# Kernel tuning notes

Hardware: AMD Instinct MI355X
Metric: run time of the kernel (lower is better)

## Reference

```python
import jax, jax.numpy as jnp
import numpy as np

D_MODEL = 1024


def pos_encoding(seq_len, d_model):
    # pos: [S,1], i: [d/2]
    pos = jnp.arange(seq_len, dtype=jnp.float32)[:, None]
    i = jnp.arange(0, d_model, 2, dtype=jnp.float32)
    angle_rates = 1.0 / jnp.power(10000.0, i / d_model)
    angle_rads = pos * angle_rates  # [S, d/2]
    # NOTE: original concatenates sin block then cos block (not interleaved)
    return jnp.concatenate([jnp.sin(angle_rads), jnp.cos(angle_rads)], axis=-1)  # [S, d]


def setup_inputs() -> dict:
    key = jax.random.key(0)
    ks = jax.random.split(key, 4)
    B, S, D = 4, 2048, D_MODEL
    scale = 1.0 / np.sqrt(D)
    x = jax.random.normal(ks[0], (B, S, D), dtype=jnp.float32)
    Wq = jax.random.normal(ks[1], (D, D), dtype=jnp.float32) * scale
    Wk = jax.random.normal(ks[2], (D, D), dtype=jnp.float32) * scale
    Wv = jax.random.normal(ks[3], (D, D), dtype=jnp.float32) * scale
    bq = jnp.zeros((D,), dtype=jnp.float32)
    bk = jnp.zeros((D,), dtype=jnp.float32)
    bv = jnp.zeros((D,), dtype=jnp.float32)
    return {"x": x, "Wq": Wq, "bq": bq, "Wk": Wk, "bk": bk, "Wv": Wv, "bv": bv}


def reference(x, Wq, bq, Wk, bk, Wv, bv):
    B, S, D = x.shape
    pe = pos_encoding(S, D)  # [S, D]
    h = x + pe[None, :, :]
    q = jnp.einsum('bsd,de->bse', h, Wq) + bq
    k = jnp.einsum('bsd,de->bse', h, Wk) + bk
    v = jnp.einsum('bsd,de->bse', h, Wv) + bv
    logits = jnp.einsum('bqd,bkd->bqk', q, k) / jnp.sqrt(jnp.float32(D))
    attn = jax.nn.softmax(logits, axis=-1)
    out = jnp.einsum('bqk,bkd->bqd', attn, v)
    return x + out
```

## Files before the change

### kernel.cpp

```cpp
#include <hip/hip_runtime.h>
#include <stdint.h>


#define AS1(p) ((__attribute__((address_space(1))) void*)(p))
#define AS3(p) ((__attribute__((address_space(3))) void*)(p))

typedef _Float16 f16x8 __attribute__((ext_vector_type(8)));
typedef _Float16 f16x4 __attribute__((ext_vector_type(4)));
typedef float f32x4 __attribute__((ext_vector_type(4)));

__global__ __launch_bounds__(256) void prep(const float* __restrict__ x,
                                            _Float16* __restrict__ h,
                                            const float* __restrict__ Wq,
                                            const float* __restrict__ Wk,
                                            const float* __restrict__ Wv,
                                            _Float16* __restrict__ Wt,
                                            float* __restrict__ rowsum) {
  const int bx = blockIdx.x;
  const int tid = threadIdx.x;
  if (bx < 8192) {
    const size_t e = ((size_t)bx * 256 + tid) * 4;
    const int d = (int)(e & 1023);
    const int s = (int)((e >> 10) & 2047);
    const float4 xv = *(const float4*)(x + e);
    const int half = d >> 9;
    const int j0 = d & 511;
    const float c = -0.017988946039016f;
    f16x4 o;
#pragma unroll
    for (int t = 0; t < 4; t++) {
      const float r = __expf((float)(j0 + t) * c);
      const float a = (float)s * r;
      const float p = half ? __cosf(a) : __sinf(a);
      const float xe = (t == 0) ? xv.x : (t == 1) ? xv.y : (t == 2) ? xv.z : xv.w;
      o[t] = (_Float16)(xe + p);
    }
    *(f16x4*)(h + e) = o;
  } else if (bx < 11264) {
    __shared__ float t[32][33];
    const int w = bx - 8192;
    const int z = w >> 10;
    const int rem = w & 1023;
    const int n0 = (rem & 31) * 32, k0 = (rem >> 5) * 32;
    const float* W = (z == 0) ? Wq : (z == 1) ? Wk : Wv;
    _Float16* o = Wt + (size_t)z * 1048576;
    const int tx = tid & 31, ty = tid >> 5;
#pragma unroll
    for (int i = ty; i < 32; i += 8)
      t[i][tx] = W[(size_t)(k0 + i) * 1024 + (n0 + tx)];
    __syncthreads();
#pragma unroll
    for (int i = ty; i < 32; i += 8)
      o[(size_t)(n0 + i) * 1024 + (k0 + tx)] = (_Float16)t[tx][i];
  } else {
    rowsum[(bx - 11264) * 256 + tid] = 0.f;
  }
}

template <int MODE, int NBUF>
__global__ __launch_bounds__(256) void gemm_bt(
    const _Float16* __restrict__ A0, long long sA,
    const _Float16* __restrict__ B0, long long sB,
    void* __restrict__ C0, long long sC,
    const float* __restrict__ aux0, const float* __restrict__ aux1,
    const float* __restrict__ aux2, float* __restrict__ rowsum,
    _Float16* __restrict__ vT,
    long long sX, const int K, const int N, const int ldc) {
  __shared__ __align__(16) _Float16 As[NBUF * 128 * 32];
  __shared__ __align__(16) _Float16 Bs[NBUF * 128 * 32];
  const int tid = threadIdx.x;
  const int bid = blockIdx.x;

  int z, bm0, bn0;
  if (MODE == 0) {
    const int c = bid & 7, t = bid >> 3;
    const int mhi = t & 7, u = t >> 3;
    bm0 = (mhi * 8 + c) * 128;
    bn0 = (u & 7) * 128;
    z = u >> 3;
  } else if (MODE == 1) {
    const int c = bid & 7, t = bid >> 3;
    const int zx = (t & 7) * 8 + c;
    const int y = t >> 3;
    z = zx >> 4; bm0 = (zx & 15) * 128; bn0 = y * 128;
  } else {
    const int c = bid & 7, t = bid >> 3;
    const int zx = (t & 3) * 8 + c;
    const int y = t >> 2;
    z = zx >> 3; bm0 = (zx & 7) * 128; bn0 = y * 128;
  }
  const _Float16* A = A0 + (size_t)z * sA;
  const _Float16* Bt = B0 + (size_t)z * sB;

  const _Float16* a0 = A + (size_t)(bm0 + (tid >> 2)) * K + (tid & 3) * 8;
  const _Float16* a1 = a0 + (size_t)64 * K;
  const _Float16* b0 = Bt + (size_t)(bn0 + (tid >> 2)) * K + (tid & 3) * 8;
  const _Float16* b1 = b0 + (size_t)64 * K;

  const int lane = tid & 63, wave = tid >> 6;
  const int wr = wave >> 1, wc = wave & 1;
  const int quad = lane >> 4, l16 = lane & 15;

  f32x4 acc[4][4];
#pragma unroll
  for (int i = 0; i < 4; i++)
#pragma unroll
    for (int j = 0; j < 4; j++) {
      f32x4 zz = {0.f, 0.f, 0.f, 0.f};
      acc[i][j] = zz;
    }

  for (int k0 = 0; k0 < K; k0 += 32 * NBUF) {
    __syncthreads();
#pragma unroll
    for (int u = 0; u < NBUF; u++) {
      __builtin_amdgcn_global_load_lds(AS1(a0 + k0 + u * 32),
                                       AS3(&As[u * 4096 + tid * 8]), 16, 0, 0);
      __builtin_amdgcn_global_load_lds(AS1(a1 + k0 + u * 32),
                                       AS3(&As[u * 4096 + tid * 8 + 2048]), 16, 0, 0);
      __builtin_amdgcn_global_load_lds(AS1(b0 + k0 + u * 32),
                                       AS3(&Bs[u * 4096 + tid * 8]), 16, 0, 0);
      __builtin_amdgcn_global_load_lds(AS1(b1 + k0 + u * 32),
                                       AS3(&Bs[u * 4096 + tid * 8 + 2048]), 16, 0, 0);
    }
    __syncthreads();
#pragma unroll
    for (int u = 0; u < NBUF; u++) {
      f16x8 af[4], bfr[4];
#pragma unroll
      for (int i = 0; i < 4; i++)
        af[i] = *(const f16x8*)&As[u * 4096 + (wr * 64 + i * 16 + l16) * 32 + quad * 8];
#pragma unroll
      for (int j = 0; j < 4; j++)
        bfr[j] = *(const f16x8*)&Bs[u * 4096 + (wc * 64 + j * 16 + l16) * 32 + quad * 8];
#pragma unroll
      for (int i = 0; i < 4; i++)
#pragma unroll
        for (int j = 0; j < 4; j++)
          acc[i][j] = __builtin_amdgcn_mfma_f32_16x16x32_f16(af[i], bfr[j],
                                                             acc[i][j], 0, 0, 0);
    }
  }

  const int rowb = bm0 + wr * 64 + quad * 4;
  const int colb = bn0 + wc * 64 + l16;
  if (MODE == 0) {
    const float* bias = (z == 0) ? aux0 : (z == 1) ? aux1 : aux2;
    if (z == 2) {
      const int b = rowb >> 11, sl = rowb & 2047;
      _Float16* vb = vT + (size_t)b * 2097152;
#pragma unroll
      for (int i = 0; i < 4; i++)
#pragma unroll
        for (int j = 0; j < 4; j++) {
          const int gn = colb + j * 16;
          const float bb = bias[gn];
          f16x4 o;
#pragma unroll
          for (int r = 0; r < 4; r++) o[r] = (_Float16)(acc[i][j][r] + bb);
          *(f16x4*)&vb[(size_t)gn * 2048 + sl + i * 16] = o;
        }
    } else {
      _Float16* C = (_Float16*)C0 + (size_t)z * sC;
#pragma unroll
      for (int i = 0; i < 4; i++)
#pragma unroll
        for (int j = 0; j < 4; j++) {
          const int gn = colb + j * 16;
          const float bb = bias[gn];
#pragma unroll
          for (int r = 0; r < 4; r++)
            C[(size_t)(rowb + i * 16 + r) * N + gn] = (_Float16)(acc[i][j][r] + bb);
        }
    }
  } else if (MODE == 1) {
    _Float16* C = (_Float16*)C0 + (size_t)z * sC;
    float rs[4] = {0.f, 0.f, 0.f, 0.f};
#pragma unroll
    for (int i = 0; i < 4; i++)
#pragma unroll
      for (int j = 0; j < 4; j++) {
        const int gn = colb + j * 16;
        f16x4 o;
        float pj = 0.f;
#pragma unroll
        for (int r = 0; r < 4; r++) {
          const float e = __expf(acc[i][j][r] * 0.03125f);
          o[r] = (_Float16)e;
          pj += e;
        }
        rs[j] += pj;
        *(f16x4*)&C[(size_t)gn * ldc + rowb + i * 16] = o;
      }
#pragma unroll
    for (int j = 0; j < 4; j++) {
      float v = rs[j];
      v += __shfl_xor(v, 16);
      v += __shfl_xor(v, 32);
      if (quad == 0) atomicAdd(&rowsum[z * 2048 + colb + j * 16], v);
    }
  } else {
    float* C = (float*)C0 + (size_t)z * sC;
    const float* X = aux0 + (size_t)z * sX;
    float inv[4];
#pragma unroll
    for (int j = 0; j < 4; j++)
      inv[j] = 1.0f / rowsum[z * 2048 + colb + j * 16];
#pragma unroll
    for (int i = 0; i < 4; i++)
#pragma unroll
      for (int j = 0; j < 4; j++) {
        const int gn = colb + j * 16;
        const size_t base = (size_t)gn * ldc + rowb + i * 16;
        const float4 xv = *(const float4*)(X + base);
        float4 o;
        o.x = acc[i][j][0] * inv[j] + xv.x;
        o.y = acc[i][j][1] * inv[j] + xv.y;
        o.z = acc[i][j][2] * inv[j] + xv.z;
        o.w = acc[i][j][3] * inv[j] + xv.w;
        *(float4*)(C + base) = o;
      }
  }
}

extern "C" void kernel_launch(void* const* d_in, const int* in_sizes, int n_in,
                              void* d_out, int out_size, void* d_ws, size_t ws_size,
                              hipStream_t stream) {
  (void)in_sizes; (void)n_in; (void)out_size; (void)ws_size;
  const float* x  = (const float*)d_in[0];
  const float* Wq = (const float*)d_in[1];
  const float* bq = (const float*)d_in[2];
  const float* Wk = (const float*)d_in[3];
  const float* bk = (const float*)d_in[4];
  const float* Wv = (const float*)d_in[5];
  const float* bv = (const float*)d_in[6];
  float* out = (float*)d_out;
  char* ws = (char*)d_ws;

  _Float16* h    = (_Float16*)(ws);
  _Float16* Wt   = (_Float16*)(ws + 16777216);
  _Float16* qkv  = (_Float16*)(ws + 23068672);
  _Float16* attn = (_Float16*)(ws + 73400320);
  float* rowsum  = (float*)   (ws + 106954752);

  const long long E = 8388608;
  _Float16* vT = qkv + 2 * E;

  prep<<<11296, 256, 0, stream>>>(x, h, Wq, Wk, Wv, Wt, rowsum);

  gemm_bt<0, 1><<<1536, 256, 0, stream>>>(
      h, 0LL, Wt, 1048576LL, qkv, E, bq, bk, bv, nullptr, vT,
      0LL, 1024, 1024, 0);

  gemm_bt<1, 2><<<1024, 256, 0, stream>>>(
      qkv + E, 2097152LL, qkv, 2097152LL, attn, 4194304LL,
      nullptr, nullptr, nullptr, rowsum, nullptr,
      0LL, 1024, 2048, 2048);

  gemm_bt<2, 2><<<512, 256, 0, stream>>>(
      vT, 2097152LL, attn, 4194304LL, out, 2097152LL,
      x, nullptr, nullptr, rowsum, nullptr,
      2097152LL, 2048, 2048, 1024);
}
```

Measured before the change: 281.9 us.

## Use 256x256 tiles, 8 waves and double-buffered prefetch for QKV and QK GEMMs

Replaces the 128x128, 4-wave GEMM for the QKV projection and QK^T/exp stages with a 256x256-tile, 512-thread kernel. The new kernel double-buffers LDS, issues async global-to-LDS loads for future k-steps while the MFMAs run, and uses explicit waitcnt, barriers and setprio to overlap copies with compute. The PV stage is split into its own kernel that keeps the old tiling. The larger tiles raise data reuse per block but use much more LDS and more registers, which lowers occupancy. Only 256 or 384 blocks are launched, which may not spread evenly across CUs.

Measured after the change: 271.8 us. -3.6%, faster.

```diff
diff --git a/kernel.cpp b/kernel.cpp
--- a/kernel.cpp
+++ b/kernel.cpp
@@ -57,38 +57,184 @@
   }
 }
 
-template <int MODE, int NBUF>
-__global__ __launch_bounds__(256) void gemm_bt(
+template <int MODE>
+__global__ __launch_bounds__(512) void gemm8p(
     const _Float16* __restrict__ A0, long long sA,
     const _Float16* __restrict__ B0, long long sB,
     void* __restrict__ C0, long long sC,
     const float* __restrict__ aux0, const float* __restrict__ aux1,
     const float* __restrict__ aux2, float* __restrict__ rowsum,
-    _Float16* __restrict__ vT,
-    long long sX, const int K, const int N, const int ldc) {
-  __shared__ __align__(16) _Float16 As[NBUF * 128 * 32];
-  __shared__ __align__(16) _Float16 Bs[NBUF * 128 * 32];
+    _Float16* __restrict__ vT, const int K, const int N, const int ldc) {
+  __shared__ __align__(16) _Float16 As[2][2][8192];
+  __shared__ __align__(16) _Float16 Bs[2][2][8192];
   const int tid = threadIdx.x;
   const int bid = blockIdx.x;
 
   int z, bm0, bn0;
   if (MODE == 0) {
-    const int c = bid & 7, t = bid >> 3;
-    const int mhi = t & 7, u = t >> 3;
-    bm0 = (mhi * 8 + c) * 128;
-    bn0 = (u & 7) * 128;
-    z = u >> 3;
-  } else if (MODE == 1) {
-    const int c = bid & 7, t = bid >> 3;
-    const int zx = (t & 7) * 8 + c;
-    const int y = t >> 3;
-    z = zx >> 4; bm0 = (zx & 15) * 128; bn0 = y * 128;
+    const int w = (bid & 7) * 48 + (bid >> 3);
+    const int m = w / 12, r = w - m * 12;
+    z = r >> 2; bn0 = (r & 3) * 256; bm0 = m * 256;
   } else {
-    const int c = bid & 7, t = bid >> 3;
-    const int zx = (t & 3) * 8 + c;
-    const int y = t >> 2;
-    z = zx >> 3; bm0 = (zx & 7) * 128; bn0 = y * 128;
-  }
+    const int w = (bid & 7) * 32 + (bid >> 3);
+    z = w >> 6;
+    const int r = w & 63;
+    bm0 = (r >> 3) * 256; bn0 = (r & 7) * 256;
+  }
+  const _Float16* A = A0 + (size_t)z * sA;
+  const _Float16* Bt = B0 + (size_t)z * sB;
+
+  const _Float16* aS = A + (size_t)(bm0 + (tid >> 2)) * K + (tid & 3) * 8;
+  const _Float16* bS = Bt + (size_t)(bn0 + (tid >> 2)) * K + (tid & 3) * 8;
+  const size_t half = (size_t)128 * K;
+
+  auto stage = [&](int kt, int q) {
+    const int b = kt & 1;
+    _Float16* ad = &As[b][q][tid * 8];
+    _Float16* bd = &Bs[b][q][tid * 8];
+    const _Float16* ag = aS + kt * 64 + q * 32;
+    const _Float16* bg = bS + kt * 64 + q * 32;
+    __builtin_amdgcn_global_load_lds(AS1(ag), AS3(ad), 16, 0, 0);
+    __builtin_amdgcn_global_load_lds(AS1(ag + half), AS3(ad + 4096), 16, 0, 0);
+    __builtin_amdgcn_global_load_lds(AS1(bg), AS3(bd), 16, 0, 0);
+    __builtin_amdgcn_global_load_lds(AS1(bg + half), AS3(bd + 4096), 16, 0, 0);
+  };
+
+  const int lane = tid & 63, wave = tid >> 6;
+  const int wr = wave >> 2, wc = wave & 3;
+  const int quad = lane >> 4, l16 = lane & 15;
+
+  f32x4 acc[8][4];
+#pragma unroll
+  for (int i = 0; i < 8; i++)
+#pragma unroll
+    for (int j = 0; j < 4; j++) {
+      f32x4 zz = {0.f, 0.f, 0.f, 0.f};
+      acc[i][j] = zz;
+    }
+
+  const int nt = K >> 6;
+
+  stage(0, 0); stage(0, 1); stage(1, 0);
+  asm volatile("s_waitcnt vmcnt(8)" ::: "memory");
+  __builtin_amdgcn_s_barrier();
+
+  for (int t = 0; t < nt; ++t) {
+    const int b = t & 1;
+#pragma unroll
+    for (int q = 0; q < 2; ++q) {
+      f16x8 af[8], bf[4];
+#pragma unroll
+      for (int i = 0; i < 8; i++)
+        af[i] = *(const f16x8*)&As[b][q][(wr * 128 + i * 16 + l16) * 32 + quad * 8];
+#pragma unroll
+      for (int j = 0; j < 4; j++)
+        bf[j] = *(const f16x8*)&Bs[b][q][(wc * 64 + j * 16 + l16) * 32 + quad * 8];
+      if (q == 0) { if (t + 1 < nt) stage(t + 1, 1); }
+      else        { if (t + 2 < nt) stage(t + 2, 0); }
+      __builtin_amdgcn_s_barrier();
+      asm volatile("s_waitcnt lgkmcnt(0)" ::: "memory");
+      __builtin_amdgcn_sched_barrier(0);
+      __builtin_amdgcn_s_setprio(1);
+#pragma unroll
+      for (int i = 0; i < 8; i++)
+#pragma unroll
+        for (int j = 0; j < 4; j++)
+          acc[i][j] = __builtin_amdgcn_mfma_f32_16x16x32_f16(af[i], bf[j],
+                                                             acc[i][j], 0, 0, 0);
+      __builtin_amdgcn_s_setprio(0);
+      __builtin_amdgcn_sched_barrier(0);
+      const bool last = (t == nt - 1) && (q == 1);
+      if (!last) {
+        if (q == 0) {
+          if (t + 1 < nt) asm volatile("s_waitcnt vmcnt(8)" ::: "memory");
+          else            asm volatile("s_waitcnt vmcnt(0)" ::: "memory");
+        } else {
+          if (t + 3 <= nt) asm volatile("s_waitcnt vmcnt(8)" ::: "memory");
+          else             asm volatile("s_waitcnt vmcnt(4)" ::: "memory");
+        }
+        __builtin_amdgcn_s_barrier();
+      }
+    }
+  }
+
+  const int rowb = bm0 + wr * 128 + quad * 4;
+  const int colb = bn0 + wc * 64 + l16;
+  if (MODE == 0) {
+    const float* bias = (z == 0) ? aux0 : (z == 1) ? aux1 : aux2;
+    if (z == 2) {
+      const int bb_ = rowb >> 11, sl = rowb & 2047;
+      _Float16* vb = vT + (size_t)bb_ * 2097152;
+#pragma unroll
+      for (int i = 0; i < 8; i++)
+#pragma unroll
+        for (int j = 0; j < 4; j++) {
+          const int gn = colb + j * 16;
+          const float bb = bias[gn];
+          f16x4 o;
+#pragma unroll
+          for (int r = 0; r < 4; r++) o[r] = (_Float16)(acc[i][j][r] + bb);
+          *(f16x4*)&vb[(size_t)gn * 2048 + sl + i * 16] = o;
+        }
+    } else {
+      _Float16* C = (_Float16*)C0 + (size_t)z * sC;
+#pragma unroll
+      for (int i = 0; i < 8; i++)
+#pragma unroll
+        for (int j = 0; j < 4; j++) {
+          const int gn = colb + j * 16;
+          const float bb = bias[gn];
+#pragma unroll
+          for (int r = 0; r < 4; r++)
+            C[(size_t)(rowb + i * 16 + r) * N + gn] = (_Float16)(acc[i][j][r] + bb);
+        }
+    }
+  } else {
+    _Float16* C = (_Float16*)C0 + (size_t)z * sC;
+    float rs[4] = {0.f, 0.f, 0.f, 0.f};
+#pragma unroll
+    for (int i = 0; i < 8; i++)
+#pragma unroll
+      for (int j = 0; j < 4; j++) {
+        const int gn = colb + j * 16;
+        f16x4 o;
+        float pj = 0.f;
+#pragma unroll
+        for (int r = 0; r < 4; r++) {
+          const float e = __expf(acc[i][j][r] * 0.03125f);
+          o[r] = (_Float16)e;
+          pj += e;
+        }
+        rs[j] += pj;
+        *(f16x4*)&C[(size_t)gn * ldc + rowb + i * 16] = o;
+      }
+#pragma unroll
+    for (int j = 0; j < 4; j++) {
+      float v = rs[j];
+      v += __shfl_xor(v, 16);
+      v += __shfl_xor(v, 32);
+      if (quad == 0) atomicAdd(&rowsum[z * 2048 + colb + j * 16], v);
+    }
+  }
+}
+
+__global__ __launch_bounds__(256) void gemm_pv(
+    const _Float16* __restrict__ A0, long long sA,
+    const _Float16* __restrict__ B0, long long sB,
+    float* __restrict__ C0, long long sC,
+    const float* __restrict__ X0, const float* __restrict__ rowsum,
+    long long sX, const int K, const int ldc) {
+  __shared__ __align__(16) _Float16 As[2 * 128 * 32];
+  __shared__ __align__(16) _Float16 Bs[2 * 128 * 32];
+  const int tid = threadIdx.x;
+  const int bid = blockIdx.x;
+
+  const int c = bid & 7, t0 = bid >> 3;
+  const int zx = (t0 & 3) * 8 + c;
+  const int y = t0 >> 2;
+  const int z = zx >> 3;
+  const int bm0 = (zx & 7) * 128, bn0 = y * 128;
+
   const _Float16* A = A0 + (size_t)z * sA;
   const _Float16* Bt = B0 + (size_t)z * sB;
 
@@ -110,10 +256,10 @@
       acc[i][j] = zz;
     }
 
-  for (int k0 = 0; k0 < K; k0 += 32 * NBUF) {
+  for (int k0 = 0; k0 < K; k0 += 64) {
     __syncthreads();
 #pragma unroll
-    for (int u = 0; u < NBUF; u++) {
+    for (int u = 0; u < 2; u++) {
       __builtin_amdgcn_global_load_lds(AS1(a0 + k0 + u * 32),
                                        AS3(&As[u * 4096 + tid * 8]), 16, 0, 0);
       __builtin_amdgcn_global_load_lds(AS1(a1 + k0 + u * 32),
@@ -125,7 +271,7 @@
     }
     __syncthreads();
 #pragma unroll
-    for (int u = 0; u < NBUF; u++) {
+    for (int u = 0; u < 2; u++) {
       f16x8 af[4], bfr[4];
 #pragma unroll
       for (int i = 0; i < 4; i++)
@@ -144,83 +290,26 @@
 
   const int rowb = bm0 + wr * 64 + quad * 4;
   const int colb = bn0 + wc * 64 + l16;
-  if (MODE == 0) {
-    const float* bias = (z == 0) ? aux0 : (z == 1) ? aux1 : aux2;
-    if (z == 2) {
-      const int b = rowb >> 11, sl = rowb & 2047;
-      _Float16* vb = vT + (size_t)b * 2097152;
-#pragma unroll
-      for (int i = 0; i < 4; i++)
-#pragma unroll
-        for (int j = 0; j < 4; j++) {
-          const int gn = colb + j * 16;
-          const float bb = bias[gn];
-          f16x4 o;
-#pragma unroll
-          for (int r = 0; r < 4; r++) o[r] = (_Float16)(acc[i][j][r] + bb);
-          *(f16x4*)&vb[(size_t)gn * 2048 + sl + i * 16] = o;
-        }
-    } else {
-      _Float16* C = (_Float16*)C0 + (size_t)z * sC;
-#pragma unroll
-      for (int i = 0; i < 4; i++)
-#pragma unroll
-        for (int j = 0; j < 4; j++) {
-          const int gn = colb + j * 16;
-          const float bb = bias[gn];
-#pragma unroll
-          for (int r = 0; r < 4; r++)
-            C[(size_t)(rowb + i * 16 + r) * N + gn] = (_Float16)(acc[i][j][r] + bb);
-        }
-    }
-  } else if (MODE == 1) {
-    _Float16* C = (_Float16*)C0 + (size_t)z * sC;
-    float rs[4] = {0.f, 0.f, 0.f, 0.f};
-#pragma unroll
-    for (int i = 0; i < 4; i++)
-#pragma unroll
-      for (int j = 0; j < 4; j++) {
-        const int gn = colb + j * 16;
-        f16x4 o;
-        float pj = 0.f;
-#pragma unroll
-        for (int r = 0; r < 4; r++) {
-          const float e = __expf(acc[i][j][r] * 0.03125f);
-          o[r] = (_Float16)e;
-          pj += e;
-        }
-        rs[j] += pj;
-        *(f16x4*)&C[(size_t)gn * ldc + rowb + i * 16] = o;
-      }
+  float* C = C0 + (size_t)z * sC;
+  const float* X = X0 + (size_t)z * sX;
+  float inv[4];
+#pragma unroll
+  for (int j = 0; j < 4; j++)
+    inv[j] = 1.0f / rowsum[z * 2048 + colb + j * 16];
+#pragma unroll
+  for (int i = 0; i < 4; i++)
 #pragma unroll
     for (int j = 0; j < 4; j++) {
-      float v = rs[j];
-      v += __shfl_xor(v, 16);
-      v += __shfl_xor(v, 32);
-      if (quad == 0) atomicAdd(&rowsum[z * 2048 + colb + j * 16], v);
-    }
-  } else {
-    float* C = (float*)C0 + (size_t)z * sC;
-    const float* X = aux0 + (size_t)z * sX;
-    float inv[4];
-#pragma unroll
-    for (int j = 0; j < 4; j++)
-      inv[j] = 1.0f / rowsum[z * 2048 + colb + j * 16];
-#pragma unroll
-    for (int i = 0; i < 4; i++)
-#pragma unroll
-      for (int j = 0; j < 4; j++) {
-        const int gn = colb + j * 16;
-        const size_t base = (size_t)gn * ldc + rowb + i * 16;
-        const float4 xv = *(const float4*)(X + base);
-        float4 o;
-        o.x = acc[i][j][0] * inv[j] + xv.x;
-        o.y = acc[i][j][1] * inv[j] + xv.y;
-        o.z = acc[i][j][2] * inv[j] + xv.z;
-        o.w = acc[i][j][3] * inv[j] + xv.w;
-        *(float4*)(C + base) = o;
-      }
-  }
+      const int gn = colb + j * 16;
+      const size_t base = (size_t)gn * ldc + rowb + i * 16;
+      const float4 xv = *(const float4*)(X + base);
+      float4 o;
+      o.x = acc[i][j][0] * inv[j] + xv.x;
+      o.y = acc[i][j][1] * inv[j] + xv.y;
+      o.z = acc[i][j][2] * inv[j] + xv.z;
+      o.w = acc[i][j][3] * inv[j] + xv.w;
+      *(float4*)(C + base) = o;
+    }
 }
 
 extern "C" void kernel_launch(void* const* d_in, const int* in_sizes, int n_in,
@@ -248,17 +337,16 @@
 
   prep<<<11296, 256, 0, stream>>>(x, h, Wq, Wk, Wv, Wt, rowsum);
 
-  gemm_bt<0, 1><<<1536, 256, 0, stream>>>(
+  gemm8p<0><<<384, 512, 0, stream>>>(
       h, 0LL, Wt, 1048576LL, qkv, E, bq, bk, bv, nullptr, vT,
-      0LL, 1024, 1024, 0);
-
-  gemm_bt<1, 2><<<1024, 256, 0, stream>>>(
+      1024, 1024, 0);
+
+  gemm8p<1><<<256, 512, 0, stream>>>(
       qkv + E, 2097152LL, qkv, 2097152LL, attn, 4194304LL,
       nullptr, nullptr, nullptr, rowsum, nullptr,
-      0LL, 1024, 2048, 2048);
-
-  gemm_bt<2, 2><<<512, 256, 0, stream>>>(
+      1024, 2048, 2048);
+
+  gemm_pv<<<512, 256, 0, stream>>>(
       vT, 2097152LL, attn, 4194304LL, out, 2097152LL,
-      x, nullptr, nullptr, rowsum, nullptr,
-      2097152LL, 2048, 2048, 1024);
+      x, rowsum, 2097152LL, 2048, 1024);
 }
```

## Pipeline GEMM k-loop with 4-slot LDS ring and 3-stage-ahead async loads

Applied to the files above, without the earlier changes.

Replaces the load-all-then-compute loop with a 4-slot LDS ring buffer. Global-to-LDS loads run three k-steps ahead, tracked with explicit vmcnt waits and one barrier per step. The MFMA block is raised in priority with s_setprio, and sched barriers fence it off. This aims to hide global memory latency behind matrix math, at the cost of 64KB of LDS per block, which may reduce occupancy.

New measurement: 266.7 us. 1.06x faster.

```diff
diff --git a/kernel.cpp b/kernel.cpp
--- a/kernel.cpp
+++ b/kernel.cpp
@@ -57,7 +57,7 @@
   }
 }
 
-template <int MODE, int NBUF>
+template <int MODE>
 __global__ __launch_bounds__(256) void gemm_bt(
     const _Float16* __restrict__ A0, long long sA,
     const _Float16* __restrict__ B0, long long sB,
@@ -66,8 +66,8 @@
     const float* __restrict__ aux2, float* __restrict__ rowsum,
     _Float16* __restrict__ vT,
     long long sX, const int K, const int N, const int ldc) {
-  __shared__ __align__(16) _Float16 As[NBUF * 128 * 32];
-  __shared__ __align__(16) _Float16 Bs[NBUF * 128 * 32];
+  __shared__ __align__(16) _Float16 As[4 * 4096];
+  __shared__ __align__(16) _Float16 Bs[4 * 4096];
   const int tid = threadIdx.x;
   const int bid = blockIdx.x;
 
@@ -97,6 +97,15 @@
   const _Float16* b0 = Bt + (size_t)(bn0 + (tid >> 2)) * K + (tid & 3) * 8;
   const _Float16* b1 = b0 + (size_t)64 * K;
 
+  auto stage = [&](int s) {
+    const int r = s & 3;
+    const int k = s * 32;
+    __builtin_amdgcn_global_load_lds(AS1(a0 + k), AS3(&As[r * 4096 + tid * 8]), 16, 0, 0);
+    __builtin_amdgcn_global_load_lds(AS1(a1 + k), AS3(&As[r * 4096 + tid * 8 + 2048]), 16, 0, 0);
+    __builtin_amdgcn_global_load_lds(AS1(b0 + k), AS3(&Bs[r * 4096 + tid * 8]), 16, 0, 0);
+    __builtin_amdgcn_global_load_lds(AS1(b1 + k), AS3(&Bs[r * 4096 + tid * 8 + 2048]), 16, 0, 0);
+  };
+
   const int lane = tid & 63, wave = tid >> 6;
   const int wr = wave >> 1, wc = wave & 1;
   const int quad = lane >> 4, l16 = lane & 15;
@@ -110,35 +119,39 @@
       acc[i][j] = zz;
     }
 
-  for (int k0 = 0; k0 < K; k0 += 32 * NBUF) {
-    __syncthreads();
-#pragma unroll
-    for (int u = 0; u < NBUF; u++) {
-      __builtin_amdgcn_global_load_lds(AS1(a0 + k0 + u * 32),
-                                       AS3(&As[u * 4096 + tid * 8]), 16, 0, 0);
-      __builtin_amdgcn_global_load_lds(AS1(a1 + k0 + u * 32),
-                                       AS3(&As[u * 4096 + tid * 8 + 2048]), 16, 0, 0);
-      __builtin_amdgcn_global_load_lds(AS1(b0 + k0 + u * 32),
-                                       AS3(&Bs[u * 4096 + tid * 8]), 16, 0, 0);
-      __builtin_amdgcn_global_load_lds(AS1(b1 + k0 + u * 32),
-                                       AS3(&Bs[u * 4096 + tid * 8 + 2048]), 16, 0, 0);
-    }
-    __syncthreads();
-#pragma unroll
-    for (int u = 0; u < NBUF; u++) {
-      f16x8 af[4], bfr[4];
-#pragma unroll
-      for (int i = 0; i < 4; i++)
-        af[i] = *(const f16x8*)&As[u * 4096 + (wr * 64 + i * 16 + l16) * 32 + quad * 8];
+  const int NS = K >> 5;
+
+  stage(0); stage(1); stage(2);
+  asm volatile("s_waitcnt vmcnt(8)" ::: "memory");
+  __builtin_amdgcn_s_barrier();
+
+  for (int s = 0; s < NS; ++s) {
+    const int r = s & 3;
+    f16x8 af[4], bf[4];
+#pragma unroll
+    for (int i = 0; i < 4; i++)
+      af[i] = *(const f16x8*)&As[r * 4096 + (wr * 64 + i * 16 + l16) * 32 + quad * 8];
+#pragma unroll
+    for (int j = 0; j < 4; j++)
+      bf[j] = *(const f16x8*)&Bs[r * 4096 + (wc * 64 + j * 16 + l16) * 32 + quad * 8];
+    if (s + 3 < NS) stage(s + 3);
+    __builtin_amdgcn_s_barrier();
+    asm volatile("s_waitcnt lgkmcnt(0)" ::: "memory");
+    __builtin_amdgcn_sched_barrier(0);
+    __builtin_amdgcn_s_setprio(1);
+#pragma unroll
+    for (int i = 0; i < 4; i++)
 #pragma unroll
       for (int j = 0; j < 4; j++)
-        bfr[j] = *(const f16x8*)&Bs[u * 4096 + (wc * 64 + j * 16 + l16) * 32 + quad * 8];
-#pragma unroll
-      for (int i = 0; i < 4; i++)
-#pragma unroll
-        for (int j = 0; j < 4; j++)
-          acc[i][j] = __builtin_amdgcn_mfma_f32_16x16x32_f16(af[i], bfr[j],
-                                                             acc[i][j], 0, 0, 0);
+        acc[i][j] = __builtin_amdgcn_mfma_f32_16x16x32_f16(af[i], bf[j],
+                                                           acc[i][j], 0, 0, 0);
+    __builtin_amdgcn_s_setprio(0);
+    __builtin_amdgcn_sched_barrier(0);
+    if (s + 1 < NS) {
+      if (s + 3 < NS)       asm volatile("s_waitcnt vmcnt(8)" ::: "memory");
+      else if (s + 3 == NS) asm volatile("s_waitcnt vmcnt(4)" ::: "memory");
+      else                  asm volatile("s_waitcnt vmcnt(0)" ::: "memory");
+      __builtin_amdgcn_s_barrier();
     }
   }
 
@@ -248,16 +261,16 @@
 
   prep<<<11296, 256, 0, stream>>>(x, h, Wq, Wk, Wv, Wt, rowsum);
 
-  gemm_bt<0, 1><<<1536, 256, 0, stream>>>(
+  gemm_bt<0><<<1536, 256, 0, stream>>>(
       h, 0LL, Wt, 1048576LL, qkv, E, bq, bk, bv, nullptr, vT,
       0LL, 1024, 1024, 0);
 
-  gemm_bt<1, 2><<<1024, 256, 0, stream>>>(
+  gemm_bt<1><<<1024, 256, 0, stream>>>(
       qkv + E, 2097152LL, qkv, 2097152LL, attn, 4194304LL,
       nullptr, nullptr, nullptr, rowsum, nullptr,
       0LL, 1024, 2048, 2048);
 
-  gemm_bt<2, 2><<<512, 256, 0, stream>>>(
+  gemm_bt<2><<<512, 256, 0, stream>>>(
       vT, 2097152LL, attn, 4194304LL, out, 2097152LL,
       x, nullptr, nullptr, rowsum, nullptr,
       2097152LL, 2048, 2048, 1024);
```
